# Performance work log

Measured on AMD Instinct MI355X. Metric: run time of the kernel, lower is better.

The kernel has to match this reference:

```python
import jax, jax.numpy as jnp
import numpy as np

B, S, D, H = 512, 64, 1024, 16  # seq_len=64 fixed by Reshape([-1,8,8,d_model])
DH = D // H


def setup_inputs() -> dict:
    key = jax.random.key(0)
    ks = jax.random.split(key, 5)
    w_scale = 0.02  # keep pre-softmax logits / activations in a sane range
    return {
        "x": jax.random.normal(ks[0], (B, S, D), jnp.float32),
        "wq_w": jax.random.normal(ks[1], (D, D), jnp.float32) * w_scale,
        "wq_b": jnp.zeros((D,), jnp.float32),
        "wk_w": jax.random.normal(ks[2], (D, D), jnp.float32) * w_scale,
        "wk_b": jnp.zeros((D,), jnp.float32),
        "wv_w": jax.random.normal(ks[3], (D, D), jnp.float32) * w_scale,
        "wv_b": jnp.zeros((D,), jnp.float32),
        "wo_w": jax.random.normal(ks[4], (D, D), jnp.float32) * w_scale,
        "wo_b": jnp.zeros((D,), jnp.float32),
    }


def _split_heads(t):
    # [B, S, D] -> [B, H, S, DH]
    b, s, _ = t.shape
    return t.reshape(b, s, H, DH).transpose(0, 2, 1, 3)


def reference(x, wq_w, wq_b, wk_w, wk_b, wv_w, wv_b, wo_w, wo_b):
    b, s, d = x.shape
    q = _split_heads(x @ wq_w + wq_b)
    k = _split_heads(x @ wk_w + wk_b)
    v = _split_heads(x @ wv_w + wv_b)
    # NOTE: original scales by sqrt(d_model), not sqrt(depth)
    scores = jnp.einsum("bhqd,bhkd->bhqk", q, k) / jnp.sqrt(jnp.float32(d))
    # original 'padding mask': (scores == 0) * 1e-9 added to scores
    scores = scores + (scores == 0).astype(scores.dtype) * 1e-9
    attn = jax.nn.softmax(scores, axis=-1)
    ctx = jnp.einsum("bhqk,bhkd->bhqd", attn, v)  # [B, H, S, DH]
    ctx = ctx.transpose(0, 2, 1, 3).reshape(b, s, d)  # [B, S, D]
    # keras Dense(..., activation='gelu') uses exact (erf) gelu by default
    out = jax.nn.gelu(ctx @ wo_w + wo_b, approximate=False)
    # Reshape([-1, 8, 8, D]) then squeeze -> [B, 8, 8, D]
    return out.reshape(b, 8, 8, d)
```

## Files before the change

### kernel.cpp

```cpp
#include <hip/hip_runtime.h>
#include <cstdint>
#include <math.h>

typedef float f32x4 __attribute__((ext_vector_type(4)));
typedef __bf16 bf16x8 __attribute__((ext_vector_type(8)));
typedef unsigned short u16x8 __attribute__((ext_vector_type(8)));
typedef unsigned short u16x4 __attribute__((ext_vector_type(4)));

typedef __attribute__((address_space(1))) const void* gas_cvptr;
typedef __attribute__((address_space(3))) void* las_vptr;

#define WAITV12 asm volatile("s_waitcnt vmcnt(12)" ::: "memory")
#define WAITV8 asm volatile("s_waitcnt vmcnt(8)" ::: "memory")
#define WAITV4 asm volatile("s_waitcnt vmcnt(4)" ::: "memory")
#define WAITV0 asm volatile("s_waitcnt vmcnt(0)" ::: "memory")
#define WAITL0 asm volatile("s_waitcnt lgkmcnt(0)" ::: "memory")
#define SB()   __builtin_amdgcn_sched_barrier(0)
#define BAR()  __builtin_amdgcn_s_barrier()

__device__ __forceinline__ unsigned short f32_to_bf16(float f) {
  uint32_t u = __builtin_bit_cast(uint32_t, f);
  u += 0x7FFFu + ((u >> 16) & 1u);
  return (unsigned short)(u >> 16);
}

__device__ __forceinline__ bf16x8 ld_bf16x8(const unsigned short* p) {
  return __builtin_bit_cast(bf16x8, *(const u16x8*)p);
}

__global__ void cvt_x(const float* __restrict__ x, unsigned short* __restrict__ xb, int n4) {
  int stride = gridDim.x * blockDim.x;
  for (int i = blockIdx.x * blockDim.x + threadIdx.x; i < n4; i += stride) {
    float4 v = ((const float4*)x)[i];
    u16x4 o = { f32_to_bf16(v.x), f32_to_bf16(v.y), f32_to_bf16(v.z), f32_to_bf16(v.w) };
    ((u16x4*)xb)[i] = o;
  }
}

__global__ void cvt_w(const float* __restrict__ wq, const float* __restrict__ wk,
                      const float* __restrict__ wv, const float* __restrict__ wo,
                      unsigned short* __restrict__ wqkvT, unsigned short* __restrict__ woT) {
  const int z = blockIdx.z;
  const float* __restrict__ w = (z == 0) ? wq : (z == 1) ? wk : (z == 2) ? wv : wo;
  unsigned short* __restrict__ out = (z < 3) ? (wqkvT + (size_t)z * 1024 * 1024) : woT;
  __shared__ float tile[64][65];
  const int r0 = blockIdx.y * 64;
  const int c0 = blockIdx.x * 64;
  const int t = threadIdx.x;
#pragma unroll
  for (int i = 0; i < 4; i++) {
    int row = (t >> 4) + i * 16;
    int col = (t & 15) * 4;
    float4 v = *(const float4*)&w[(size_t)(r0 + row) * 1024 + c0 + col];
    tile[row][col] = v.x; tile[row][col + 1] = v.y;
    tile[row][col + 2] = v.z; tile[row][col + 3] = v.w;
  }
  __syncthreads();
#pragma unroll
  for (int i = 0; i < 2; i++) {
    int nr = (t >> 3) + i * 32;
    int kc = (t & 7) * 8;
    u16x8 o;
#pragma unroll
    for (int j = 0; j < 8; j++) o[j] = f32_to_bf16(tile[kc + j][nr]);
    *(u16x8*)&out[(size_t)(c0 + nr) * 1024 + r0 + kc] = o;
  }
}

struct Frags { bf16x8 afA[4], bfr[4], afB[4]; };

__device__ __forceinline__ void read_frags(Frags& f, const unsigned short* ab,
                                           const unsigned short* bb, int aRow0,
                                           int bRow0, int li, int koff) {
#pragma unroll
  for (int m = 0; m < 4; m++) f.afA[m] = ld_bf16x8(ab + (aRow0 + m * 16 + li) * 32 + koff);
#pragma unroll
  for (int n = 0; n < 4; n++) f.bfr[n] = ld_bf16x8(bb + (bRow0 + n * 16 + li) * 32 + koff);
#pragma unroll
  for (int m = 0; m < 4; m++)
    f.afB[m] = ld_bf16x8(ab + (aRow0 + 64 + m * 16 + li) * 32 + koff);
}

template <int EPI>
__global__ __launch_bounds__(512, 2) void gemm256(
    const unsigned short* __restrict__ A, const unsigned short* __restrict__ Bt,
    const float* __restrict__ b0, const float* __restrict__ b1, const float* __restrict__ b2,
    unsigned short* __restrict__ Qb, unsigned short* __restrict__ Kb, unsigned short* __restrict__ Vb,
    float* __restrict__ Out, int Ncols, int K) {
  __shared__ __align__(16) unsigned short As[4][256][32];
  __shared__ __align__(16) unsigned short Bs[4][256][32];
  const int NT = K >> 5;
  const int nb = Ncols >> 8;
  const int nwg = gridDim.x;
  const int cpx = nwg >> 3;
  const int bid = blockIdx.x;
  const int wg = (bid & 7) * cpx + (bid >> 3);
  const int tm = wg / nb, tn = wg % nb;
  const int rowBase = tm << 8, colBase = tn << 8;
  const int t = threadIdx.x;
  const int lane = t & 63;
  const int w = t >> 6;
  const int li = lane & 15, lg = lane >> 4;
  const int wm = w >> 2, wn = w & 3;
  const int aRow0 = wm * 128;
  const int bRow0 = wn * 64;
  const int koff = ((lg ^ ((li >> 1) & 3)) << 3);

  const int c0 = t, c1 = t + 512;
  const int r0s = c0 >> 2, r1s = c1 >> 2;
  const int l0s = (c0 & 3) ^ ((r0s >> 1) & 3);
  const int l1s = (c1 & 3) ^ ((r1s >> 1) & 3);
  const unsigned short* gA0 = A + (size_t)(rowBase + r0s) * K + l0s * 8;
  const unsigned short* gA1 = A + (size_t)(rowBase + r1s) * K + l1s * 8;
  const unsigned short* gB0 = Bt + (size_t)(colBase + r0s) * K + l0s * 8;
  const unsigned short* gB1 = Bt + (size_t)(colBase + r1s) * K + l1s * 8;

#define STAGE_AB(tile_) do { int b_ = (tile_) & 3; int kt_ = (tile_) << 5;                    \
    __builtin_amdgcn_global_load_lds((gas_cvptr)(gA0 + kt_),                                  \
        (las_vptr)(&As[b_][0][0] + c0 * 8), 16, 0, 0);                                        \
    __builtin_amdgcn_global_load_lds((gas_cvptr)(gA1 + kt_),                                  \
        (las_vptr)(&As[b_][0][0] + c1 * 8), 16, 0, 0);                                        \
    __builtin_amdgcn_global_load_lds((gas_cvptr)(gB0 + kt_),                                  \
        (las_vptr)(&Bs[b_][0][0] + c0 * 8), 16, 0, 0);                                        \
    __builtin_amdgcn_global_load_lds((gas_cvptr)(gB1 + kt_),                                  \
        (las_vptr)(&Bs[b_][0][0] + c1 * 8), 16, 0, 0); } while (0)

  STAGE_AB(0); STAGE_AB(1); STAGE_AB(2); STAGE_AB(3);
  WAITV12;
  BAR();

  f32x4 acc[8][4] = {};
  Frags F0, F1;
  read_frags(F0, &As[0][0][0], &Bs[0][0][0], aRow0, bRow0, li, koff);

#define TILE_BODY(tt_, CUR, NXT) do {                                                         \
    WAITL0; SB();                                                                             \
    __builtin_amdgcn_s_setprio(1);                                                            \
    _Pragma("unroll")                                                                         \
    for (int m = 0; m < 4; m++)                                                               \
      _Pragma("unroll")                                                                       \
      for (int n = 0; n < 4; n++)                                                             \
        acc[m][n] = __builtin_amdgcn_mfma_f32_16x16x32_bf16(CUR.afA[m], CUR.bfr[n],           \
                                                            acc[m][n], 0, 0, 0);              \
    __builtin_amdgcn_s_setprio(0);                                                            \
    if ((tt_) <= NT - 4)      WAITV8;                                                         \
    else if ((tt_) == NT - 3) WAITV4;                                                         \
    else if ((tt_) == NT - 2) WAITV0;                                                         \
    BAR();                                                                                    \
    if ((tt_) + 1 < NT)                                                                       \
      read_frags(NXT, &As[((tt_) + 1) & 3][0][0], &Bs[((tt_) + 1) & 3][0][0],                 \
                 aRow0, bRow0, li, koff);                                                     \
    if ((tt_) + 4 < NT) STAGE_AB((tt_) + 4);                                                  \
    __builtin_amdgcn_s_setprio(1);                                                            \
    _Pragma("unroll")                                                                         \
    for (int m = 0; m < 4; m++)                                                               \
      _Pragma("unroll")                                                                       \
      for (int n = 0; n < 4; n++)                                                             \
        acc[4 + m][n] = __builtin_amdgcn_mfma_f32_16x16x32_bf16(CUR.afB[m], CUR.bfr[n],       \
                                                                acc[4 + m][n], 0, 0, 0);      \
    __builtin_amdgcn_s_setprio(0);                                                            \
  } while (0)

  for (int tt = 0; tt < NT; tt += 2) {
    TILE_BODY(tt, F0, F1);
    TILE_BODY(tt + 1, F1, F0);
  }
#undef TILE_BODY
#undef STAGE_AB

  if (EPI == 0) {
    const int part = colBase >> 10;
    const float* __restrict__ bias = (part == 0) ? b0 : (part == 1) ? b1 : b2;
    unsigned short* __restrict__ dst = (part == 0) ? Qb : (part == 1) ? Kb : Vb;
#pragma unroll
    for (int mi = 0; mi < 8; mi++) {
      const int rowb = rowBase + aRow0 + mi * 16 + lg * 4;
#pragma unroll
      for (int r = 0; r < 4; r++) {
        const int row = rowb + r;
        const int b = row >> 6, s = row & 63;
#pragma unroll
        for (int n = 0; n < 4; n++) {
          const int col = colBase + bRow0 + n * 16 + li;
          const int within = col & 1023;
          const int h = within >> 6, dh = within & 63;
          float v = acc[mi][n][r] + bias[within];
          dst[(size_t)((b * 16 + h) * 64 + s) * 64 + dh] = f32_to_bf16(v);
        }
      }
    }
  } else {
#pragma unroll
    for (int mi = 0; mi < 8; mi++) {
      const int rowb = rowBase + aRow0 + mi * 16 + lg * 4;
#pragma unroll
      for (int r = 0; r < 4; r++) {
#pragma unroll
        for (int n = 0; n < 4; n++) {
          const int col = colBase + bRow0 + n * 16 + li;
          float v = acc[mi][n][r] + b0[col];
          v = 0.5f * v * (1.0f + erff(v * 0.70710678118654752f));
          Out[(size_t)(rowb + r) * 1024 + col] = v;
        }
      }
    }
  }
}

__global__ __launch_bounds__(256) void attn(
    const unsigned short* __restrict__ Qb, const unsigned short* __restrict__ Kb,
    const unsigned short* __restrict__ Vb, unsigned short* __restrict__ ctx) {
  __shared__ __align__(16) unsigned short Qs[64][72];
  __shared__ __align__(16) unsigned short Ks[64][72];
  __shared__ __align__(16) unsigned short Vt[64][72];
  __shared__ __align__(16) unsigned short Ps[64][72];
  const int bh = blockIdx.x;
  const int b = bh >> 4, h = bh & 15;
  const int t = threadIdx.x, lane = t & 63, w = t >> 6;
  const int li = lane & 15, lg = lane >> 4;
  const unsigned short* __restrict__ Qg = Qb + (size_t)bh * 4096;
  const unsigned short* __restrict__ Kg = Kb + (size_t)bh * 4096;
  const unsigned short* __restrict__ Vg = Vb + (size_t)bh * 4096;

#pragma unroll
  for (int i = 0; i < 2; i++) {
    const int c = t + i * 256;
    const int row = c >> 3, col8 = (c & 7) * 8;
    *(u16x8*)&Qs[row][col8] = *(const u16x8*)&Qg[row * 64 + col8];
    *(u16x8*)&Ks[row][col8] = *(const u16x8*)&Kg[row * 64 + col8];
    u16x8 v = *(const u16x8*)&Vg[row * 64 + col8];
#pragma unroll
    for (int j = 0; j < 8; j++) Vt[col8 + j][row] = v[j];
  }
  __syncthreads();

  f32x4 sc[4] = {};
#pragma unroll
  for (int ks = 0; ks < 2; ks++) {
    bf16x8 qa = ld_bf16x8(&Qs[w * 16 + li][ks * 32 + lg * 8]);
#pragma unroll
    for (int n = 0; n < 4; n++) {
      bf16x8 kf = ld_bf16x8(&Ks[n * 16 + li][ks * 32 + lg * 8]);
      sc[n] = __builtin_amdgcn_mfma_f32_16x16x32_bf16(qa, kf, sc[n], 0, 0, 0);
    }
  }

#pragma unroll
  for (int r = 0; r < 4; r++) {
    float v0 = sc[0][r] * 0.03125f, v1 = sc[1][r] * 0.03125f;
    float v2 = sc[2][r] * 0.03125f, v3 = sc[3][r] * 0.03125f;
    float mx = fmaxf(fmaxf(v0, v1), fmaxf(v2, v3));
#pragma unroll
    for (int off = 1; off < 16; off <<= 1) mx = fmaxf(mx, __shfl_xor(mx, off, 64));
    float e0 = __expf(v0 - mx), e1 = __expf(v1 - mx);
    float e2 = __expf(v2 - mx), e3 = __expf(v3 - mx);
    float sum = e0 + e1 + e2 + e3;
#pragma unroll
    for (int off = 1; off < 16; off <<= 1) sum += __shfl_xor(sum, off, 64);
    float is = 1.0f / sum;
    const int q = w * 16 + lg * 4 + r;
    Ps[q][0 * 16 + li] = f32_to_bf16(e0 * is);
    Ps[q][1 * 16 + li] = f32_to_bf16(e1 * is);
    Ps[q][2 * 16 + li] = f32_to_bf16(e2 * is);
    Ps[q][3 * 16 + li] = f32_to_bf16(e3 * is);
  }
  __syncthreads();

  f32x4 oc[4] = {};
#pragma unroll
  for (int ks = 0; ks < 2; ks++) {
    bf16x8 pa = ld_bf16x8(&Ps[w * 16 + li][ks * 32 + lg * 8]);
#pragma unroll
    for (int n = 0; n < 4; n++) {
      bf16x8 vf = ld_bf16x8(&Vt[n * 16 + li][ks * 32 + lg * 8]);
      oc[n] = __builtin_amdgcn_mfma_f32_16x16x32_bf16(pa, vf, oc[n], 0, 0, 0);
    }
  }
#pragma unroll
  for (int n = 0; n < 4; n++)
#pragma unroll
    for (int r = 0; r < 4; r++)
      ctx[(size_t)(b * 64 + w * 16 + lg * 4 + r) * 1024 + h * 64 + n * 16 + li] =
          f32_to_bf16(oc[n][r]);
}

extern "C" void kernel_launch(void* const* d_in, const int* in_sizes, int n_in,
                              void* d_out, int out_size, void* d_ws, size_t ws_size,
                              hipStream_t stream) {
  const float* x  = (const float*)d_in[0];
  const float* wq = (const float*)d_in[1];
  const float* bq = (const float*)d_in[2];
  const float* wk = (const float*)d_in[3];
  const float* bk = (const float*)d_in[4];
  const float* wv = (const float*)d_in[5];
  const float* bv = (const float*)d_in[6];
  const float* wo = (const float*)d_in[7];
  const float* bo = (const float*)d_in[8];
  float* out = (float*)d_out;

  const int D = 1024;
  const int M = in_sizes[0] / D;

  char* ws = (char*)d_ws;
  unsigned short* xb    = (unsigned short*)ws;
  unsigned short* wqkvT = (unsigned short*)(ws + (size_t)M * 1024 * 2);
  unsigned short* woT   = wqkvT + (size_t)3 * 1024 * 1024;
  unsigned short* Qb    = woT + (size_t)1024 * 1024;
  unsigned short* Kb    = Qb + (size_t)M * 1024;
  unsigned short* Vb    = Kb + (size_t)M * 1024;
  unsigned short* ctx   = xb;

  cvt_x<<<2048, 256, 0, stream>>>(x, xb, M * D / 4);
  cvt_w<<<dim3(16, 16, 4), 256, 0, stream>>>(wq, wk, wv, wo, wqkvT, woT);
  gemm256<0><<<(M / 256) * (3072 / 256), 512, 0, stream>>>(
      xb, wqkvT, bq, bk, bv, Qb, Kb, Vb, nullptr, 3072, 1024);
  attn<<<(M / 64) * 16, 256, 0, stream>>>(Qb, Kb, Vb, ctx);
  gemm256<1><<<(M / 256) * (1024 / 256), 512, 0, stream>>>(
      ctx, woT, bo, nullptr, nullptr, nullptr, nullptr, nullptr, out, 1024, 1024);
}
```

Before: 409.8 us.

## Assign one attention head per wavefront and load Q/K directly into registers

The attention kernel now processes four (batch, head) pairs per block, one per wavefront, so each wave computes a full 64x64 score tile and output instead of a 16-row slice. Q and K fragments are loaded straight from global memory into registers, and only V (transposed) and P go through per-wave shared memory, which removes both block-wide barriers. The aim is to cut LDS traffic and synchronisation. In exchange, register pressure rises (16 accumulator tiles plus the fragments), fewer blocks are launched, and the uncoalesced per-lane global fragment loads may cost bandwidth.

```diff
diff --git a/kernel.cpp b/kernel.cpp
--- a/kernel.cpp
+++ b/kernel.cpp
@@ -210,78 +210,91 @@
 __global__ __launch_bounds__(256) void attn(
     const unsigned short* __restrict__ Qb, const unsigned short* __restrict__ Kb,
     const unsigned short* __restrict__ Vb, unsigned short* __restrict__ ctx) {
-  __shared__ __align__(16) unsigned short Qs[64][72];
-  __shared__ __align__(16) unsigned short Ks[64][72];
-  __shared__ __align__(16) unsigned short Vt[64][72];
-  __shared__ __align__(16) unsigned short Ps[64][72];
-  const int bh = blockIdx.x;
-  const int b = bh >> 4, h = bh & 15;
+  __shared__ __align__(16) unsigned short VtA[4][64][72];
+  __shared__ __align__(16) unsigned short PsA[4][64][72];
   const int t = threadIdx.x, lane = t & 63, w = t >> 6;
   const int li = lane & 15, lg = lane >> 4;
+  const int bh = (blockIdx.x << 2) | w;
+  const int b = bh >> 4, h = bh & 15;
   const unsigned short* __restrict__ Qg = Qb + (size_t)bh * 4096;
   const unsigned short* __restrict__ Kg = Kb + (size_t)bh * 4096;
   const unsigned short* __restrict__ Vg = Vb + (size_t)bh * 4096;
-
-#pragma unroll
-  for (int i = 0; i < 2; i++) {
-    const int c = t + i * 256;
-    const int row = c >> 3, col8 = (c & 7) * 8;
-    *(u16x8*)&Qs[row][col8] = *(const u16x8*)&Qg[row * 64 + col8];
-    *(u16x8*)&Ks[row][col8] = *(const u16x8*)&Kg[row * 64 + col8];
+  unsigned short (* __restrict__ Vt)[72] = VtA[w];
+  unsigned short (* __restrict__ Ps)[72] = PsA[w];
+
+#pragma unroll
+  for (int i = 0; i < 8; i++) {
+    const int c = lane + (i << 6);
+    const int row = c >> 3, col8 = (c & 7) << 3;
     u16x8 v = *(const u16x8*)&Vg[row * 64 + col8];
 #pragma unroll
     for (int j = 0; j < 8; j++) Vt[col8 + j][row] = v[j];
   }
-  __syncthreads();
-
-  f32x4 sc[4] = {};
+
+  bf16x8 qa[4][2], kf[4][2];
+#pragma unroll
+  for (int m = 0; m < 4; m++)
+#pragma unroll
+    for (int ks = 0; ks < 2; ks++) {
+      qa[m][ks] = ld_bf16x8(&Qg[(m * 16 + li) * 64 + ks * 32 + lg * 8]);
+      kf[m][ks] = ld_bf16x8(&Kg[(m * 16 + li) * 64 + ks * 32 + lg * 8]);
+    }
+
+  f32x4 sc[4][4] = {};
+#pragma unroll
+  for (int ks = 0; ks < 2; ks++)
+#pragma unroll
+    for (int m = 0; m < 4; m++)
+#pragma unroll
+      for (int n = 0; n < 4; n++)
+        sc[m][n] = __builtin_amdgcn_mfma_f32_16x16x32_bf16(qa[m][ks], kf[n][ks],
+                                                           sc[m][n], 0, 0, 0);
+
+#pragma unroll
+  for (int m = 0; m < 4; m++)
+#pragma unroll
+    for (int r = 0; r < 4; r++) {
+      float v0 = sc[m][0][r] * 0.03125f, v1 = sc[m][1][r] * 0.03125f;
+      float v2 = sc[m][2][r] * 0.03125f, v3 = sc[m][3][r] * 0.03125f;
+      float mx = fmaxf(fmaxf(v0, v1), fmaxf(v2, v3));
+#pragma unroll
+      for (int off = 1; off < 16; off <<= 1) mx = fmaxf(mx, __shfl_xor(mx, off, 64));
+      float e0 = __expf(v0 - mx), e1 = __expf(v1 - mx);
+      float e2 = __expf(v2 - mx), e3 = __expf(v3 - mx);
+      float sum = e0 + e1 + e2 + e3;
+#pragma unroll
+      for (int off = 1; off < 16; off <<= 1) sum += __shfl_xor(sum, off, 64);
+      float is = 1.0f / sum;
+      const int q = m * 16 + lg * 4 + r;
+      Ps[q][0 + li] = f32_to_bf16(e0 * is);
+      Ps[q][16 + li] = f32_to_bf16(e1 * is);
+      Ps[q][32 + li] = f32_to_bf16(e2 * is);
+      Ps[q][48 + li] = f32_to_bf16(e3 * is);
+    }
+
+  f32x4 oc[4][4] = {};
 #pragma unroll
   for (int ks = 0; ks < 2; ks++) {
-    bf16x8 qa = ld_bf16x8(&Qs[w * 16 + li][ks * 32 + lg * 8]);
-#pragma unroll
-    for (int n = 0; n < 4; n++) {
-      bf16x8 kf = ld_bf16x8(&Ks[n * 16 + li][ks * 32 + lg * 8]);
-      sc[n] = __builtin_amdgcn_mfma_f32_16x16x32_bf16(qa, kf, sc[n], 0, 0, 0);
-    }
-  }
-
-#pragma unroll
-  for (int r = 0; r < 4; r++) {
-    float v0 = sc[0][r] * 0.03125f, v1 = sc[1][r] * 0.03125f;
-    float v2 = sc[2][r] * 0.03125f, v3 = sc[3][r] * 0.03125f;
-    float mx = fmaxf(fmaxf(v0, v1), fmaxf(v2, v3));
-#pragma unroll
-    for (int off = 1; off < 16; off <<= 1) mx = fmaxf(mx, __shfl_xor(mx, off, 64));
-    float e0 = __expf(v0 - mx), e1 = __expf(v1 - mx);
-    float e2 = __expf(v2 - mx), e3 = __expf(v3 - mx);
-    float sum = e0 + e1 + e2 + e3;
-#pragma unroll
-    for (int off = 1; off < 16; off <<= 1) sum += __shfl_xor(sum, off, 64);
-    float is = 1.0f / sum;
-    const int q = w * 16 + lg * 4 + r;
-    Ps[q][0 * 16 + li] = f32_to_bf16(e0 * is);
-    Ps[q][1 * 16 + li] = f32_to_bf16(e1 * is);
-    Ps[q][2 * 16 + li] = f32_to_bf16(e2 * is);
-    Ps[q][3 * 16 + li] = f32_to_bf16(e3 * is);
-  }
-  __syncthreads();
-
-  f32x4 oc[4] = {};
-#pragma unroll
-  for (int ks = 0; ks < 2; ks++) {
-    bf16x8 pa = ld_bf16x8(&Ps[w * 16 + li][ks * 32 + lg * 8]);
-#pragma unroll
-    for (int n = 0; n < 4; n++) {
-      bf16x8 vf = ld_bf16x8(&Vt[n * 16 + li][ks * 32 + lg * 8]);
-      oc[n] = __builtin_amdgcn_mfma_f32_16x16x32_bf16(pa, vf, oc[n], 0, 0, 0);
-    }
-  }
-#pragma unroll
-  for (int n = 0; n < 4; n++)
-#pragma unroll
-    for (int r = 0; r < 4; r++)
-      ctx[(size_t)(b * 64 + w * 16 + lg * 4 + r) * 1024 + h * 64 + n * 16 + li] =
-          f32_to_bf16(oc[n][r]);
+    bf16x8 vf[4];
+#pragma unroll
+    for (int n = 0; n < 4; n++) vf[n] = ld_bf16x8(&Vt[n * 16 + li][ks * 32 + lg * 8]);
+#pragma unroll
+    for (int m = 0; m < 4; m++) {
+      bf16x8 pa = ld_bf16x8(&Ps[m * 16 + li][ks * 32 + lg * 8]);
+#pragma unroll
+      for (int n = 0; n < 4; n++)
+        oc[m][n] = __builtin_amdgcn_mfma_f32_16x16x32_bf16(pa, vf[n], oc[m][n], 0, 0, 0);
+    }
+  }
+
+#pragma unroll
+  for (int m = 0; m < 4; m++)
+#pragma unroll
+    for (int n = 0; n < 4; n++)
+#pragma unroll
+      for (int r = 0; r < 4; r++)
+        ctx[(size_t)(b * 64 + m * 16 + lg * 4 + r) * 1024 + h * 64 + n * 16 + li] =
+            f32_to_bf16(oc[m][n][r]);
 }
 
 extern "C" void kernel_launch(void* const* d_in, const int* in_sizes, int n_in,
@@ -314,7 +327,7 @@
   cvt_w<<<dim3(16, 16, 4), 256, 0, stream>>>(wq, wk, wv, wo, wqkvT, woT);
   gemm256<0><<<(M / 256) * (3072 / 256), 512, 0, stream>>>(
       xb, wqkvT, bq, bk, bv, Qb, Kb, Vb, nullptr, 3072, 1024);
-  attn<<<(M / 64) * 16, 256, 0, stream>>>(Qb, Kb, Vb, ctx);
+  attn<<<((M / 64) * 16) / 4, 256, 0, stream>>>(Qb, Kb, Vb, ctx);
   gemm256<1><<<(M / 256) * (1024 / 256), 512, 0, stream>>>(
       ctx, woT, bo, nullptr, nullptr, nullptr, nullptr, nullptr, out, 1024, 1024);
 }
```

Result: slower. 438.7 us (+7.1%).

## Write V transposed from QKV GEMM and load attention operands directly from global

Applied to the files above, without the earlier changes.

The QKV projection epilogue now writes V in a per-head transposed [dh][s] layout with 4-wide vector stores. The attention kernel then loads Q, K and V fragments straight from global memory into registers instead of staging them through shared memory. This removes the shared-memory transpose of V, three LDS tiles and one block barrier. The __syncthreads between writing Ps and reading it was also removed even though each wave reads P rows written by other lanes of the same wave. That relies on intra-wave ordering and may be unsafe.

```diff
diff --git a/kernel.cpp b/kernel.cpp
--- a/kernel.cpp
+++ b/kernel.cpp
@@ -172,20 +172,38 @@
     const int part = colBase >> 10;
     const float* __restrict__ bias = (part == 0) ? b0 : (part == 1) ? b1 : b2;
     unsigned short* __restrict__ dst = (part == 0) ? Qb : (part == 1) ? Kb : Vb;
-#pragma unroll
-    for (int mi = 0; mi < 8; mi++) {
-      const int rowb = rowBase + aRow0 + mi * 16 + lg * 4;
-#pragma unroll
-      for (int r = 0; r < 4; r++) {
-        const int row = rowb + r;
-        const int b = row >> 6, s = row & 63;
+    if (part == 2) {
+#pragma unroll
+      for (int mi = 0; mi < 8; mi++) {
+        const int rowb = rowBase + aRow0 + mi * 16 + lg * 4;
+        const int bi = rowb >> 6, s0 = rowb & 63;
 #pragma unroll
         for (int n = 0; n < 4; n++) {
           const int col = colBase + bRow0 + n * 16 + li;
           const int within = col & 1023;
           const int h = within >> 6, dh = within & 63;
-          float v = acc[mi][n][r] + bias[within];
-          dst[(size_t)((b * 16 + h) * 64 + s) * 64 + dh] = f32_to_bf16(v);
+          const float bia = bias[within];
+          u16x4 o = { f32_to_bf16(acc[mi][n][0] + bia), f32_to_bf16(acc[mi][n][1] + bia),
+                      f32_to_bf16(acc[mi][n][2] + bia), f32_to_bf16(acc[mi][n][3] + bia) };
+          *(u16x4*)&dst[((size_t)(bi * 16 + h) * 64 + dh) * 64 + s0] = o;
+        }
+      }
+    } else {
+#pragma unroll
+      for (int mi = 0; mi < 8; mi++) {
+        const int rowb = rowBase + aRow0 + mi * 16 + lg * 4;
+#pragma unroll
+        for (int r = 0; r < 4; r++) {
+          const int row = rowb + r;
+          const int b = row >> 6, s = row & 63;
+#pragma unroll
+          for (int n = 0; n < 4; n++) {
+            const int col = colBase + bRow0 + n * 16 + li;
+            const int within = col & 1023;
+            const int h = within >> 6, dh = within & 63;
+            float v = acc[mi][n][r] + bias[within];
+            dst[(size_t)((b * 16 + h) * 64 + s) * 64 + dh] = f32_to_bf16(v);
+          }
         }
       }
     }
@@ -209,41 +227,33 @@
 
 __global__ __launch_bounds__(256) void attn(
     const unsigned short* __restrict__ Qb, const unsigned short* __restrict__ Kb,
-    const unsigned short* __restrict__ Vb, unsigned short* __restrict__ ctx) {
-  __shared__ __align__(16) unsigned short Qs[64][72];
-  __shared__ __align__(16) unsigned short Ks[64][72];
-  __shared__ __align__(16) unsigned short Vt[64][72];
+    const unsigned short* __restrict__ VTb, unsigned short* __restrict__ ctx) {
   __shared__ __align__(16) unsigned short Ps[64][72];
+  const int t = threadIdx.x, lane = t & 63, w = t >> 6;
+  const int li = lane & 15, lg = lane >> 4;
   const int bh = blockIdx.x;
   const int b = bh >> 4, h = bh & 15;
-  const int t = threadIdx.x, lane = t & 63, w = t >> 6;
-  const int li = lane & 15, lg = lane >> 4;
   const unsigned short* __restrict__ Qg = Qb + (size_t)bh * 4096;
   const unsigned short* __restrict__ Kg = Kb + (size_t)bh * 4096;
-  const unsigned short* __restrict__ Vg = Vb + (size_t)bh * 4096;
-
-#pragma unroll
-  for (int i = 0; i < 2; i++) {
-    const int c = t + i * 256;
-    const int row = c >> 3, col8 = (c & 7) * 8;
-    *(u16x8*)&Qs[row][col8] = *(const u16x8*)&Qg[row * 64 + col8];
-    *(u16x8*)&Ks[row][col8] = *(const u16x8*)&Kg[row * 64 + col8];
-    u16x8 v = *(const u16x8*)&Vg[row * 64 + col8];
-#pragma unroll
-    for (int j = 0; j < 8; j++) Vt[col8 + j][row] = v[j];
-  }
-  __syncthreads();
+  const unsigned short* __restrict__ Vg = VTb + (size_t)bh * 4096;
+
+  bf16x8 qa[2], kf[4][2], vf[4][2];
+#pragma unroll
+  for (int ks = 0; ks < 2; ks++) {
+    qa[ks] = ld_bf16x8(&Qg[(w * 16 + li) * 64 + ks * 32 + lg * 8]);
+#pragma unroll
+    for (int n = 0; n < 4; n++) {
+      kf[n][ks] = ld_bf16x8(&Kg[(n * 16 + li) * 64 + ks * 32 + lg * 8]);
+      vf[n][ks] = ld_bf16x8(&Vg[(n * 16 + li) * 64 + ks * 32 + lg * 8]);
+    }
+  }
 
   f32x4 sc[4] = {};
 #pragma unroll
-  for (int ks = 0; ks < 2; ks++) {
-    bf16x8 qa = ld_bf16x8(&Qs[w * 16 + li][ks * 32 + lg * 8]);
-#pragma unroll
-    for (int n = 0; n < 4; n++) {
-      bf16x8 kf = ld_bf16x8(&Ks[n * 16 + li][ks * 32 + lg * 8]);
-      sc[n] = __builtin_amdgcn_mfma_f32_16x16x32_bf16(qa, kf, sc[n], 0, 0, 0);
-    }
-  }
+  for (int ks = 0; ks < 2; ks++)
+#pragma unroll
+    for (int n = 0; n < 4; n++)
+      sc[n] = __builtin_amdgcn_mfma_f32_16x16x32_bf16(qa[ks], kf[n][ks], sc[n], 0, 0, 0);
 
 #pragma unroll
   for (int r = 0; r < 4; r++) {
@@ -259,23 +269,21 @@
     for (int off = 1; off < 16; off <<= 1) sum += __shfl_xor(sum, off, 64);
     float is = 1.0f / sum;
     const int q = w * 16 + lg * 4 + r;
-    Ps[q][0 * 16 + li] = f32_to_bf16(e0 * is);
-    Ps[q][1 * 16 + li] = f32_to_bf16(e1 * is);
-    Ps[q][2 * 16 + li] = f32_to_bf16(e2 * is);
-    Ps[q][3 * 16 + li] = f32_to_bf16(e3 * is);
-  }
-  __syncthreads();
+    Ps[q][0 + li] = f32_to_bf16(e0 * is);
+    Ps[q][16 + li] = f32_to_bf16(e1 * is);
+    Ps[q][32 + li] = f32_to_bf16(e2 * is);
+    Ps[q][48 + li] = f32_to_bf16(e3 * is);
+  }
 
   f32x4 oc[4] = {};
 #pragma unroll
   for (int ks = 0; ks < 2; ks++) {
     bf16x8 pa = ld_bf16x8(&Ps[w * 16 + li][ks * 32 + lg * 8]);
 #pragma unroll
-    for (int n = 0; n < 4; n++) {
-      bf16x8 vf = ld_bf16x8(&Vt[n * 16 + li][ks * 32 + lg * 8]);
-      oc[n] = __builtin_amdgcn_mfma_f32_16x16x32_bf16(pa, vf, oc[n], 0, 0, 0);
-    }
-  }
+    for (int n = 0; n < 4; n++)
+      oc[n] = __builtin_amdgcn_mfma_f32_16x16x32_bf16(pa, vf[n][ks], oc[n], 0, 0, 0);
+  }
+
 #pragma unroll
   for (int n = 0; n < 4; n++)
 #pragma unroll
```

Measured after the change: 429.7 us. 1.05x slower.

## Fuse fp32-to-bf16 input conversion into the QKV GEMM via fp32 LDS staging

Applied to the files above, without the earlier changes.

Removes the separate x conversion kernel and has the QKV GEMM load fp32 tiles of x directly into LDS, converting to bf16 with packed cvt instructions when building MFMA fragments. This eliminates one full read and write pass over the activation. In exchange the GEMM reads twice as many A bytes per tile, uses a larger fp32 LDS footprint with a 3-stage instead of 4-stage pipeline, and adds conversion ALU work in the inner loop.

```diff
diff --git a/kernel.cpp b/kernel.cpp
--- a/kernel.cpp
+++ b/kernel.cpp
@@ -12,6 +12,7 @@
 
 #define WAITV12 asm volatile("s_waitcnt vmcnt(12)" ::: "memory")
 #define WAITV8 asm volatile("s_waitcnt vmcnt(8)" ::: "memory")
+#define WAITV6 asm volatile("s_waitcnt vmcnt(6)" ::: "memory")
 #define WAITV4 asm volatile("s_waitcnt vmcnt(4)" ::: "memory")
 #define WAITV0 asm volatile("s_waitcnt vmcnt(0)" ::: "memory")
 #define WAITL0 asm volatile("s_waitcnt lgkmcnt(0)" ::: "memory")
@@ -28,13 +29,13 @@
   return __builtin_bit_cast(bf16x8, *(const u16x8*)p);
 }
 
-__global__ void cvt_x(const float* __restrict__ x, unsigned short* __restrict__ xb, int n4) {
-  int stride = gridDim.x * blockDim.x;
-  for (int i = blockIdx.x * blockDim.x + threadIdx.x; i < n4; i += stride) {
-    float4 v = ((const float4*)x)[i];
-    u16x4 o = { f32_to_bf16(v.x), f32_to_bf16(v.y), f32_to_bf16(v.z), f32_to_bf16(v.w) };
-    ((u16x4*)xb)[i] = o;
-  }
+__device__ __forceinline__ bf16x8 pack8(f32x4 a, f32x4 b) {
+  union { uint32_t w[4]; u16x8 v; } u;
+  asm("v_cvt_pk_bf16_f32 %0, %1, %2" : "=v"(u.w[0]) : "v"(a[0]), "v"(a[1]));
+  asm("v_cvt_pk_bf16_f32 %0, %1, %2" : "=v"(u.w[1]) : "v"(a[2]), "v"(a[3]));
+  asm("v_cvt_pk_bf16_f32 %0, %1, %2" : "=v"(u.w[2]) : "v"(b[0]), "v"(b[1]));
+  asm("v_cvt_pk_bf16_f32 %0, %1, %2" : "=v"(u.w[3]) : "v"(b[2]), "v"(b[3]));
+  return __builtin_bit_cast(bf16x8, u.v);
 }
 
 __global__ void cvt_w(const float* __restrict__ wq, const float* __restrict__ wk,
@@ -67,11 +68,143 @@
   }
 }
 
-struct Frags { bf16x8 afA[4], bfr[4], afB[4]; };
-
-__device__ __forceinline__ void read_frags(Frags& f, const unsigned short* ab,
-                                           const unsigned short* bb, int aRow0,
-                                           int bRow0, int li, int koff) {
+__global__ __launch_bounds__(512, 2) void gemm_qkv(
+    const float* __restrict__ X, const unsigned short* __restrict__ Bt,
+    const float* __restrict__ b0, const float* __restrict__ b1, const float* __restrict__ b2,
+    unsigned short* __restrict__ Qb, unsigned short* __restrict__ Kb, unsigned short* __restrict__ Vb,
+    int Ncols, int K) {
+  __shared__ __align__(16) float Asf[3][256 * 32];
+  __shared__ __align__(16) unsigned short Bs[3][256][32];
+  const int NT = K >> 5;
+  const int nb = Ncols >> 8;
+  const int nwg = gridDim.x;
+  const int cpx = nwg >> 3;
+  const int bid = blockIdx.x;
+  const int wg = (bid & 7) * cpx + (bid >> 3);
+  const int tm = wg / nb, tn = wg % nb;
+  const int rowBase = tm << 8, colBase = tn << 8;
+  const int t = threadIdx.x;
+  const int lane = t & 63;
+  const int w = t >> 6;
+  const int li = lane & 15, lg = lane >> 4;
+  const int wm = w >> 2, wn = w & 3;
+  const int aRow0 = wm * 128;
+  const int bRow0 = wn * 64;
+  const int koffB = ((lg ^ ((li >> 1) & 3)) << 3);
+  const int ca0 = (((2 * lg) ^ (li & 7)) << 2);
+  const int ca1 = ((((2 * lg) + 1) ^ (li & 7)) << 2);
+
+  const int cA0 = t, cA1 = t + 512, cA2 = t + 1024, cA3 = t + 1536;
+#define ASRC(c_) (X + (size_t)(rowBase + ((c_) >> 3)) * K + ((((c_) & 7) ^ (((c_) >> 3) & 7)) << 2))
+  const float* gA0 = ASRC(cA0);
+  const float* gA1 = ASRC(cA1);
+  const float* gA2 = ASRC(cA2);
+  const float* gA3 = ASRC(cA3);
+#undef ASRC
+  const int cB0 = t, cB1 = t + 512;
+  const int rB0 = cB0 >> 2, rB1 = cB1 >> 2;
+  const int lB0 = (cB0 & 3) ^ ((rB0 >> 1) & 3);
+  const int lB1 = (cB1 & 3) ^ ((rB1 >> 1) & 3);
+  const unsigned short* gB0 = Bt + (size_t)(colBase + rB0) * K + lB0 * 8;
+  const unsigned short* gB1 = Bt + (size_t)(colBase + rB1) * K + lB1 * 8;
+
+#define GLDS(s_, d_) __builtin_amdgcn_global_load_lds((gas_cvptr)(s_), (las_vptr)(d_), 16, 0, 0)
+#define STAGE(tile_) do { int b_ = (tile_) % 3; int kt_ = (tile_) << 5;                       \
+    GLDS(gA0 + kt_, &Asf[b_][0] + cA0 * 4);                                                   \
+    GLDS(gA1 + kt_, &Asf[b_][0] + cA1 * 4);                                                   \
+    GLDS(gA2 + kt_, &Asf[b_][0] + cA2 * 4);                                                   \
+    GLDS(gA3 + kt_, &Asf[b_][0] + cA3 * 4);                                                   \
+    GLDS(gB0 + kt_, &Bs[b_][0][0] + cB0 * 8);                                                 \
+    GLDS(gB1 + kt_, &Bs[b_][0][0] + cB1 * 8); } while (0)
+
+  STAGE(0); STAGE(1); STAGE(2);
+  WAITV12;
+  BAR();
+
+  f32x4 acc[8][4] = {};
+  struct Frags { bf16x8 afA[4], bfr[4], afB[4]; } F0, F1;
+
+#define READ_FRAGS(F, buf_) do {                                                              \
+    const float* ab_ = &Asf[buf_][0];                                                         \
+    const unsigned short* bb_ = &Bs[buf_][0][0];                                              \
+    _Pragma("unroll")                                                                         \
+    for (int m = 0; m < 4; m++) {                                                             \
+      const float* rp_ = ab_ + (aRow0 + m * 16 + li) * 32;                                    \
+      F.afA[m] = pack8(*(const f32x4*)(rp_ + ca0), *(const f32x4*)(rp_ + ca1));               \
+    }                                                                                         \
+    _Pragma("unroll")                                                                         \
+    for (int n = 0; n < 4; n++)                                                               \
+      F.bfr[n] = ld_bf16x8(bb_ + (bRow0 + n * 16 + li) * 32 + koffB);                         \
+    _Pragma("unroll")                                                                         \
+    for (int m = 0; m < 4; m++) {                                                             \
+      const float* rp_ = ab_ + (aRow0 + 64 + m * 16 + li) * 32;                               \
+      F.afB[m] = pack8(*(const f32x4*)(rp_ + ca0), *(const f32x4*)(rp_ + ca1));               \
+    }                                                                                         \
+  } while (0)
+
+  READ_FRAGS(F0, 0);
+
+#define TILE_BODY(tt_, CUR, NXT) do {                                                         \
+    WAITL0; SB();                                                                             \
+    __builtin_amdgcn_s_setprio(1);                                                            \
+    _Pragma("unroll")                                                                         \
+    for (int m = 0; m < 4; m++)                                                               \
+      _Pragma("unroll")                                                                       \
+      for (int n = 0; n < 4; n++)                                                             \
+        acc[m][n] = __builtin_amdgcn_mfma_f32_16x16x32_bf16(CUR.afA[m], CUR.bfr[n],           \
+                                                            acc[m][n], 0, 0, 0);              \
+    __builtin_amdgcn_s_setprio(0);                                                            \
+    if ((tt_) <= NT - 3)      WAITV6;                                                         \
+    else if ((tt_) == NT - 2) WAITV0;                                                         \
+    BAR();                                                                                    \
+    if ((tt_) + 1 < NT) READ_FRAGS(NXT, ((tt_) + 1) % 3);                                     \
+    if ((tt_) + 3 < NT) STAGE((tt_) + 3);                                                     \
+    __builtin_amdgcn_s_setprio(1);                                                            \
+    _Pragma("unroll")                                                                         \
+    for (int m = 0; m < 4; m++)                                                               \
+      _Pragma("unroll")                                                                       \
+      for (int n = 0; n < 4; n++)                                                             \
+        acc[4 + m][n] = __builtin_amdgcn_mfma_f32_16x16x32_bf16(CUR.afB[m], CUR.bfr[n],       \
+                                                                acc[4 + m][n], 0, 0, 0);      \
+    __builtin_amdgcn_s_setprio(0);                                                            \
+  } while (0)
+
+  for (int tt = 0; tt < NT; tt += 2) {
+    TILE_BODY(tt, F0, F1);
+    TILE_BODY(tt + 1, F1, F0);
+  }
+#undef TILE_BODY
+#undef READ_FRAGS
+#undef STAGE
+#undef GLDS
+
+  const int part = colBase >> 10;
+  const float* __restrict__ bias = (part == 0) ? b0 : (part == 1) ? b1 : b2;
+  unsigned short* __restrict__ dst = (part == 0) ? Qb : (part == 1) ? Kb : Vb;
+#pragma unroll
+  for (int mi = 0; mi < 8; mi++) {
+    const int rowb = rowBase + aRow0 + mi * 16 + lg * 4;
+#pragma unroll
+    for (int r = 0; r < 4; r++) {
+      const int row = rowb + r;
+      const int b = row >> 6, s = row & 63;
+#pragma unroll
+      for (int n = 0; n < 4; n++) {
+        const int col = colBase + bRow0 + n * 16 + li;
+        const int within = col & 1023;
+        const int h = within >> 6, dh = within & 63;
+        float v = acc[mi][n][r] + bias[within];
+        dst[(size_t)((b * 16 + h) * 64 + s) * 64 + dh] = f32_to_bf16(v);
+      }
+    }
+  }
+}
+
+struct FragsB { bf16x8 afA[4], bfr[4], afB[4]; };
+
+__device__ __forceinline__ void read_frags_b(FragsB& f, const unsigned short* ab,
+                                             const unsigned short* bb, int aRow0,
+                                             int bRow0, int li, int koff) {
 #pragma unroll
   for (int m = 0; m < 4; m++) f.afA[m] = ld_bf16x8(ab + (aRow0 + m * 16 + li) * 32 + koff);
 #pragma unroll
@@ -81,12 +214,9 @@
     f.afB[m] = ld_bf16x8(ab + (aRow0 + 64 + m * 16 + li) * 32 + koff);
 }
 
-template <int EPI>
-__global__ __launch_bounds__(512, 2) void gemm256(
+__global__ __launch_bounds__(512, 2) void gemm_out(
     const unsigned short* __restrict__ A, const unsigned short* __restrict__ Bt,
-    const float* __restrict__ b0, const float* __restrict__ b1, const float* __restrict__ b2,
-    unsigned short* __restrict__ Qb, unsigned short* __restrict__ Kb, unsigned short* __restrict__ Vb,
-    float* __restrict__ Out, int Ncols, int K) {
+    const float* __restrict__ b0, float* __restrict__ Out, int Ncols, int K) {
   __shared__ __align__(16) unsigned short As[4][256][32];
   __shared__ __align__(16) unsigned short Bs[4][256][32];
   const int NT = K >> 5;
@@ -130,8 +260,8 @@
   BAR();
 
   f32x4 acc[8][4] = {};
-  Frags F0, F1;
-  read_frags(F0, &As[0][0][0], &Bs[0][0][0], aRow0, bRow0, li, koff);
+  FragsB F0, F1;
+  read_frags_b(F0, &As[0][0][0], &Bs[0][0][0], aRow0, bRow0, li, koff);
 
 #define TILE_BODY(tt_, CUR, NXT) do {                                                         \
     WAITL0; SB();                                                                             \
@@ -148,8 +278,8 @@
     else if ((tt_) == NT - 2) WAITV0;                                                         \
     BAR();                                                                                    \
     if ((tt_) + 1 < NT)                                                                       \
-      read_frags(NXT, &As[((tt_) + 1) & 3][0][0], &Bs[((tt_) + 1) & 3][0][0],                 \
-                 aRow0, bRow0, li, koff);                                                     \
+      read_frags_b(NXT, &As[((tt_) + 1) & 3][0][0], &Bs[((tt_) + 1) & 3][0][0],               \
+                   aRow0, bRow0, li, koff);                                                   \
     if ((tt_) + 4 < NT) STAGE_AB((tt_) + 4);                                                  \
     __builtin_amdgcn_s_setprio(1);                                                            \
     _Pragma("unroll")                                                                         \
@@ -168,40 +298,17 @@
 #undef TILE_BODY
 #undef STAGE_AB
 
-  if (EPI == 0) {
-    const int part = colBase >> 10;
-    const float* __restrict__ bias = (part == 0) ? b0 : (part == 1) ? b1 : b2;
-    unsigned short* __restrict__ dst = (part == 0) ? Qb : (part == 1) ? Kb : Vb;
-#pragma unroll
-    for (int mi = 0; mi < 8; mi++) {
-      const int rowb = rowBase + aRow0 + mi * 16 + lg * 4;
-#pragma unroll
-      for (int r = 0; r < 4; r++) {
-        const int row = rowb + r;
-        const int b = row >> 6, s = row & 63;
-#pragma unroll
-        for (int n = 0; n < 4; n++) {
-          const int col = colBase + bRow0 + n * 16 + li;
-          const int within = col & 1023;
-          const int h = within >> 6, dh = within & 63;
-          float v = acc[mi][n][r] + bias[within];
-          dst[(size_t)((b * 16 + h) * 64 + s) * 64 + dh] = f32_to_bf16(v);
-        }
-      }
-    }
-  } else {
-#pragma unroll
-    for (int mi = 0; mi < 8; mi++) {
-      const int rowb = rowBase + aRow0 + mi * 16 + lg * 4;
-#pragma unroll
-      for (int r = 0; r < 4; r++) {
-#pragma unroll
-        for (int n = 0; n < 4; n++) {
-          const int col = colBase + bRow0 + n * 16 + li;
-          float v = acc[mi][n][r] + b0[col];
-          v = 0.5f * v * (1.0f + erff(v * 0.70710678118654752f));
-          Out[(size_t)(rowb + r) * 1024 + col] = v;
-        }
+#pragma unroll
+  for (int mi = 0; mi < 8; mi++) {
+    const int rowb = rowBase + aRow0 + mi * 16 + lg * 4;
+#pragma unroll
+    for (int r = 0; r < 4; r++) {
+#pragma unroll
+      for (int n = 0; n < 4; n++) {
+        const int col = colBase + bRow0 + n * 16 + li;
+        float v = acc[mi][n][r] + b0[col];
+        v = 0.5f * v * (1.0f + erff(v * 0.70710678118654752f));
+        Out[(size_t)(rowb + r) * 1024 + col] = v;
       }
     }
   }
@@ -302,19 +409,17 @@
   const int M = in_sizes[0] / D;
 
   char* ws = (char*)d_ws;
-  unsigned short* xb    = (unsigned short*)ws;
-  unsigned short* wqkvT = (unsigned short*)(ws + (size_t)M * 1024 * 2);
+  unsigned short* wqkvT = (unsigned short*)ws;
   unsigned short* woT   = wqkvT + (size_t)3 * 1024 * 1024;
   unsigned short* Qb    = woT + (size_t)1024 * 1024;
   unsigned short* Kb    = Qb + (size_t)M * 1024;
   unsigned short* Vb    = Kb + (size_t)M * 1024;
-  unsigned short* ctx   = xb;
-
-  cvt_x<<<2048, 256, 0, stream>>>(x, xb, M * D / 4);
+  unsigned short* ctx   = Vb + (size_t)M * 1024;
+
   cvt_w<<<dim3(16, 16, 4), 256, 0, stream>>>(wq, wk, wv, wo, wqkvT, woT);
-  gemm256<0><<<(M / 256) * (3072 / 256), 512, 0, stream>>>(
-      xb, wqkvT, bq, bk, bv, Qb, Kb, Vb, nullptr, 3072, 1024);
+  gemm_qkv<<<(M / 256) * (3072 / 256), 512, 0, stream>>>(
+      x, wqkvT, bq, bk, bv, Qb, Kb, Vb, 3072, 1024);
   attn<<<(M / 64) * 16, 256, 0, stream>>>(Qb, Kb, Vb, ctx);
-  gemm256<1><<<(M / 256) * (1024 / 256), 512, 0, stream>>>(
-      ctx, woT, bo, nullptr, nullptr, nullptr, nullptr, nullptr, out, 1024, 1024);
-}
+  gemm_out<<<(M / 256) * (1024 / 256), 512, 0, stream>>>(
+      ctx, woT, bo, out, 1024, 1024);
+}
```

Result: slower. 474.4 us (+15.8%).
